# Kernel optimization log

Hardware: AMD Instinct MI355X
Metric: run time of the kernel (lower is better)

## Reference

```python
import jax, jax.numpy as jnp
import numpy as np

EPS = 1e-5

def rmsnorm(x):
    # BitLinear pre-norm (no learnable scale), per BitNet b1.58 reference impl
    return x * jax.lax.rsqrt(jnp.mean(x * x, axis=-1, keepdims=True) + EPS)

def act_quant(x):
    # per-token absmax 8-bit quantization with straight-through estimator
    scale = 127.0 / jnp.clip(jnp.max(jnp.abs(x), axis=-1, keepdims=True), 1e-5)
    q = jnp.clip(jnp.round(x * scale), -128.0, 127.0) / scale
    return x + jax.lax.stop_gradient(q - x)

def weight_quant(w):
    # absmean ternary quantization {-1,0,1} with STE
    scale = 1.0 / jnp.clip(jnp.mean(jnp.abs(w)), 1e-5)
    q = jnp.clip(jnp.round(w * scale), -1.0, 1.0) / scale
    return w + jax.lax.stop_gradient(q - w)

def bitlinear(x, w, b):
    # x: [b, s, d_in], w: [d_out, d_in] (torch Linear layout), b: [d_out]
    xq = act_quant(rmsnorm(x))
    wq = weight_quant(w)
    return jnp.einsum('bsd,fd->bsf', xq, wq) + b

def setup_inputs() -> dict:
    key = jax.random.key(0)
    k0, k1, k2 = jax.random.split(key, 3)
    B, S, D, F = 2, 8192, 1024, 4096  # inner_dim = dim * mult = 4096
    x = jax.random.normal(k0, (B, S, D), dtype=jnp.float32)
    w1 = jax.random.normal(k1, (F, D), dtype=jnp.float32) * (1.0 / np.sqrt(D))
    b1 = jnp.zeros((F,), dtype=jnp.float32)
    w2 = jax.random.normal(k2, (D, F), dtype=jnp.float32) * (1.0 / np.sqrt(F))
    b2 = jnp.zeros((D,), dtype=jnp.float32)
    return {"x": x, "w1": w1, "b1": b1, "w2": w2, "b2": b2}

def reference(x, w1, b1, w2, b2):
    h = bitlinear(x, w1, b1)
    h = jax.nn.gelu(h, approximate=False)  # nn.GELU() default is exact
    # post_act_ln=False -> no LayerNorm; dropout p=0.0 -> identity
    return bitlinear(h, w2, b2)
```

## Files before the change

kernel.cpp:

```cpp
#include <hip/hip_runtime.h>
#include <hip/hip_bf16.h>
#include <stdint.h>

typedef int i32x4 __attribute__((ext_vector_type(4)));

__device__ __forceinline__ float blo(unsigned int u) {
  unsigned int v = u << 16; float f; __builtin_memcpy(&f, &v, 4); return f;
}
__device__ __forceinline__ float bhi(unsigned int u) {
  unsigned int v = u & 0xffff0000u; float f; __builtin_memcpy(&f, &v, 4); return f;
}
__device__ __forceinline__ int pack4q(float a, float b, float c, float d, float qm) {
  int i0 = (int)rintf(a * qm) & 255;
  int i1 = (int)rintf(b * qm) & 255;
  int i2 = (int)rintf(c * qm) & 255;
  int i3 = (int)rintf(d * qm) & 255;
  return i0 | (i1 << 8) | (i2 << 16) | (i3 << 24);
}

__device__ __forceinline__ float fast_gelu(float v) {
  float u = v * 0.70710678118654752f;
  float s = fabsf(u);
  float den = fmaf(0.3275911f, s, 1.0f);
  float t;
  asm("v_rcp_f32 %0, %1" : "=v"(t) : "v"(den));
  float p = t * fmaf(t, fmaf(t, fmaf(t, fmaf(t, 1.061405429f, -1.453152027f),
                                     1.421413741f), -0.284496736f), 0.254829592f);
  float e = fmaf(-p, __expf(-u * u), 1.0f);
  float er = copysignf(e, u);
  return 0.5f * v * (1.0f + er);
}

__global__ void k_reduce_abs2(const float* __restrict__ w1, const float* __restrict__ w2,
                              long n4, float* __restrict__ partials) {
  const int half = gridDim.x >> 1;
  const float* w = (blockIdx.x < half) ? w1 : w2;
  int b = (blockIdx.x < half) ? blockIdx.x : blockIdx.x - half;
  const float4* wv = (const float4*)w;
  float s = 0.0f;
  long stride = (long)half * blockDim.x;
  for (long i = (long)b * blockDim.x + threadIdx.x; i < n4; i += stride) {
    float4 v = wv[i];
    s += fabsf(v.x) + fabsf(v.y) + fabsf(v.z) + fabsf(v.w);
  }
  #pragma unroll
  for (int off = 32; off; off >>= 1) s += __shfl_down(s, off);
  __shared__ float sw[4];
  if ((threadIdx.x & 63) == 0) sw[threadIdx.x >> 6] = s;
  __syncthreads();
  if (threadIdx.x == 0) partials[blockIdx.x] = sw[0] + sw[1] + sw[2] + sw[3];
}

__global__ void k_finalize_scales(const float* __restrict__ p1, const float* __restrict__ p2,
                                  float* __restrict__ scales, float inv1, float inv2) {
  int t = threadIdx.x;
  float s1 = p1[t], s2 = p2[t];
  #pragma unroll
  for (int off = 32; off; off >>= 1) { s1 += __shfl_down(s1, off); s2 += __shfl_down(s2, off); }
  __shared__ float a1[4], a2[4];
  if ((t & 63) == 0) { a1[t >> 6] = s1; a2[t >> 6] = s2; }
  __syncthreads();
  if (t == 0) {
    scales[0] = fmaxf((a1[0]+a1[1]+a1[2]+a1[3]) * inv1, 1e-5f);
    scales[1] = fmaxf((a2[0]+a2[1]+a2[2]+a2[3]) * inv2, 1e-5f);
  }
}

__global__ void k_quant_w2(const float* __restrict__ w1, char* __restrict__ wq1,
                           const float* __restrict__ w2, char* __restrict__ wq2,
                           long n4, const float* __restrict__ scales) {
  const int half = gridDim.x >> 1;
  const bool first = blockIdx.x < half;
  const float* w = first ? w1 : w2;
  char* wq = first ? wq1 : wq2;
  int b = first ? blockIdx.x : blockIdx.x - half;
  float s = 1.0f / scales[first ? 0 : 1];
  const float4* wv = (const float4*)w;
  int* qv = (int*)wq;
  long stride = (long)half * blockDim.x;
  for (long i = (long)b * blockDim.x + threadIdx.x; i < n4; i += stride) {
    float4 v = wv[i];
    int b0 = (int)fminf(fmaxf(rintf(v.x * s), -1.0f), 1.0f) & 255;
    int b1 = (int)fminf(fmaxf(rintf(v.y * s), -1.0f), 1.0f) & 255;
    int b2 = (int)fminf(fmaxf(rintf(v.z * s), -1.0f), 1.0f) & 255;
    int b3 = (int)fminf(fmaxf(rintf(v.w * s), -1.0f), 1.0f) & 255;
    qv[i] = b0 | (b1 << 8) | (b2 << 16) | (b3 << 24);
  }
}

__global__ void k_actq_x(const float* __restrict__ x, char* __restrict__ xq,
                         float* __restrict__ alpha) {
  const int D = 1024;
  size_t t = blockIdx.x;
  int tid = threadIdx.x;
  const float4* row = (const float4*)(x + t * (size_t)D);
  float4 v = row[tid];
  float ss = v.x*v.x + v.y*v.y + v.z*v.z + v.w*v.w;
  float am = fmaxf(fmaxf(fabsf(v.x), fabsf(v.y)), fmaxf(fabsf(v.z), fabsf(v.w)));
  #pragma unroll
  for (int off = 32; off; off >>= 1) {
    ss += __shfl_down(ss, off);
    am = fmaxf(am, __shfl_down(am, off));
  }
  __shared__ float s_ss[4], s_am[4];
  if ((tid & 63) == 0) { s_ss[tid >> 6] = ss; s_am[tid >> 6] = am; }
  __syncthreads();
  ss = s_ss[0] + s_ss[1] + s_ss[2] + s_ss[3];
  am = fmaxf(fmaxf(s_am[0], s_am[1]), fmaxf(s_am[2], s_am[3]));
  float rms = rsqrtf(ss * (1.0f / D) + 1e-5f);
  float a   = fmaxf(am * rms, 1e-5f);
  float qs  = 127.0f / a;
  if (tid == 0) alpha[t] = a * (1.0f / 127.0f);
  int b0 = (int)fminf(fmaxf(rintf((v.x * rms) * qs), -128.0f), 127.0f) & 255;
  int b1 = (int)fminf(fmaxf(rintf((v.y * rms) * qs), -128.0f), 127.0f) & 255;
  int b2 = (int)fminf(fmaxf(rintf((v.z * rms) * qs), -128.0f), 127.0f) & 255;
  int b3 = (int)fminf(fmaxf(rintf((v.w * rms) * qs), -128.0f), 127.0f) & 255;
  ((int*)xq)[t * 256 + tid] = b0 | (b1 << 8) | (b2 << 16) | (b3 << 24);
}

__global__ void k_actq_h(__hip_bfloat16* __restrict__ h, float* __restrict__ alpha) {
  const int F = 4096;
  size_t t = blockIdx.x;
  int tid = threadIdx.x;
  char* rb = (char*)(h + t * (size_t)F);
  const uint4* row = (const uint4*)rb;
  uint4 u0 = row[tid], u1 = row[tid + 256];
  unsigned int uu[8] = {u0.x, u0.y, u0.z, u0.w, u1.x, u1.y, u1.z, u1.w};
  float f[16];
  #pragma unroll
  for (int i = 0; i < 8; i++) {
    f[2*i]   = fast_gelu(blo(uu[i]));
    f[2*i+1] = fast_gelu(bhi(uu[i]));
  }
  float ss = 0.0f, am = 0.0f;
  #pragma unroll
  for (int i = 0; i < 16; i++) { ss += f[i] * f[i]; am = fmaxf(am, fabsf(f[i])); }
  #pragma unroll
  for (int off = 32; off; off >>= 1) {
    ss += __shfl_down(ss, off);
    am = fmaxf(am, __shfl_down(am, off));
  }
  __shared__ float s_ss[4], s_am[4];
  if ((tid & 63) == 0) { s_ss[tid >> 6] = ss; s_am[tid >> 6] = am; }
  __syncthreads();
  ss = s_ss[0] + s_ss[1] + s_ss[2] + s_ss[3];
  am = fmaxf(fmaxf(s_am[0], s_am[1]), fmaxf(s_am[2], s_am[3]));
  float rms = rsqrtf(ss * (1.0f / F) + 1e-5f);
  float a   = fmaxf(am * rms, 1e-5f);
  float qm  = rms * (127.0f / a);
  if (tid == 0) alpha[t] = a * (1.0f / 127.0f);
  uint2 w0, w1;
  w0.x = (unsigned)pack4q(f[0],  f[1],  f[2],  f[3],  qm);
  w0.y = (unsigned)pack4q(f[4],  f[5],  f[6],  f[7],  qm);
  w1.x = (unsigned)pack4q(f[8],  f[9],  f[10], f[11], qm);
  w1.y = (unsigned)pack4q(f[12], f[13], f[14], f[15], qm);
  *(uint2*)(rb + 8 * tid) = w0;
  *(uint2*)(rb + 2048 + 8 * tid) = w1;
}

#define GLD16(GP, LP) __builtin_amdgcn_global_load_lds( \
    (__attribute__((address_space(1))) void*)(GP), \
    (__attribute__((address_space(3))) void*)(LP), 16, 0, 0)
#define VMCNT3 asm volatile("s_waitcnt vmcnt(3)" ::: "memory")
#define VMCNT0 asm volatile("s_waitcnt vmcnt(0)" ::: "memory")
#define LGKM0  do { asm volatile("s_waitcnt lgkmcnt(0)" ::: "memory"); __builtin_amdgcn_sched_barrier(0); } while(0)

template<int EPI>
__global__ __launch_bounds__(512, 4) void k_gemm_i8(
    const char* __restrict__ A, int lda,
    const char* __restrict__ B,
    const float* __restrict__ bias, const float* __restrict__ alpha,
    const float* __restrict__ scales, int which,
    void* __restrict__ Cout, int N, int K, int lgnbx)
{
  __shared__ __align__(16) char lA[3 * 8192];
  __shared__ __align__(16) char lB[3 * 16384];
  const int tid = threadIdx.x, lane = tid & 63, wid = tid >> 6;
  const int wm = wid >> 2, wn = wid & 3;
  const int nwg = gridDim.x, bid = blockIdx.x;
  const int swz = (bid & 7) * (nwg >> 3) + (bid >> 3);
  const int bx = swz & ((1 << lgnbx) - 1), by = swz >> lgnbx;
  const int m0 = by * 128, n0 = bx * 256;
  const int NT = K >> 6;

  const int srow = tid >> 2, slot = tid & 3;
  const int sswz = (slot ^ ((srow >> 1) & 3)) * 16;
  const char* gA0 = A + (size_t)(m0 +       srow) * lda + sswz;
  const char* gB0 = B + (size_t)(n0 +       srow) * K   + sswz;
  const char* gB1 = B + (size_t)(n0 + 128 + srow) * K   + sswz;
  const int ldst = srow * 64 + slot * 16;

  const int lr = lane & 15;
  const int kx = ((lane >> 4) ^ ((lane >> 1) & 3)) * 16;
  const int aoff = (wm * 64 + lr) * 64 + kx;
  const int boff = (wn * 64 + lr) * 64 + kx;

  GLD16(gA0,      lA + ldst);
  GLD16(gB0,      lB + ldst);
  GLD16(gB1,      lB + 8192 + ldst);
  GLD16(gA0 + 64, lA + 8192 + ldst);
  GLD16(gB0 + 64, lB + 16384 + ldst);
  GLD16(gB1 + 64, lB + 16384 + 8192 + ldst);

  i32x4 acc[4][4] = {};
  int cur = 0, nx1 = 1, nx2 = 2;
  for (int t = 0; t < NT; ++t) {
    const bool pf = (t + 2 < NT);
    if (t + 1 < NT) { VMCNT3; } else { VMCNT0; }
    __builtin_amdgcn_s_barrier();
    const char* pa = lA + cur * 8192 + aoff;
    const char* pb = lB + cur * 16384 + boff;
    i32x4 av[4], bv[4];
    {
      av[0] = *(const i32x4*)(pa);
      av[1] = *(const i32x4*)(pa + 1024);
      #pragma unroll
      for (int n = 0; n < 4; ++n) bv[n] = *(const i32x4*)(pb + n * 1024);
      if (pf) {
        GLD16(gA0 + 64 * (t + 2), lA + nx2 * 8192 + ldst);
        GLD16(gB0 + 64 * (t + 2), lB + nx2 * 16384 + ldst);
      }
      __builtin_amdgcn_s_barrier();
      LGKM0;
      __builtin_amdgcn_s_setprio(1);
      #pragma unroll
      for (int j = 0; j < 2; ++j)
        #pragma unroll
        for (int n = 0; n < 4; ++n)
          acc[j][n] = __builtin_amdgcn_mfma_i32_16x16x64_i8(av[j], bv[n], acc[j][n], 0, 0, 0);
      __builtin_amdgcn_s_setprio(0);
      __builtin_amdgcn_s_barrier();
    }
    {
      av[2] = *(const i32x4*)(pa + 2048);
      av[3] = *(const i32x4*)(pa + 3072);
      if (pf) GLD16(gB1 + 64 * (t + 2), lB + nx2 * 16384 + 8192 + ldst);
      LGKM0;
      __builtin_amdgcn_s_setprio(1);
      #pragma unroll
      for (int j = 2; j < 4; ++j)
        #pragma unroll
        for (int n = 0; n < 4; ++n)
          acc[j][n] = __builtin_amdgcn_mfma_i32_16x16x64_i8(av[j], bv[n], acc[j][n], 0, 0, 0);
      __builtin_amdgcn_s_setprio(0);
    }
    int tmp = cur; cur = nx1; nx1 = nx2; nx2 = tmp;
  }

  const float wdq = scales[which];
  const int lq4 = (lane >> 4) * 4;
  #pragma unroll
  for (int m = 0; m < 4; ++m) {
    const int rowb = m0 + wm * 64 + m * 16 + lq4;
    float al[4];
    #pragma unroll
    for (int q = 0; q < 4; ++q) al[q] = alpha[rowb + q] * wdq;
    #pragma unroll
    for (int n = 0; n < 4; ++n) {
      const int col = n0 + wn * 64 + n * 16 + lr;
      const float bb = bias[col];
      #pragma unroll
      for (int q = 0; q < 4; ++q) {
        float v = (float)acc[m][n][q] * al[q] + bb;
        if constexpr (EPI == 0) {
          ((__hip_bfloat16*)Cout)[(size_t)(rowb + q) * N + col] = __float2bfloat16(v);
        } else {
          ((float*)Cout)[(size_t)(rowb + q) * N + col] = v;
        }
      }
    }
  }
}

extern "C" void kernel_launch(void* const* d_in, const int* in_sizes, int n_in,
                              void* d_out, int out_size, void* d_ws, size_t ws_size,
                              hipStream_t stream) {
  const float* x  = (const float*)d_in[0];
  const float* w1 = (const float*)d_in[1];
  const float* b1 = (const float*)d_in[2];
  const float* w2 = (const float*)d_in[3];
  const float* b2 = (const float*)d_in[4];
  const int  F = in_sizes[2];
  const int  D = in_sizes[4];
  const long T = (long)in_sizes[0] / D;
  const long nW = (long)F * D;

  char* ws = (char*)d_ws;
  float* partials = (float*)ws;
  float* scales   = partials + 512;
  float* alpha1 = (float*)(ws + 4096);
  float* alpha2 = alpha1 + T;
  size_t off = 4096 + 2 * (size_t)T * sizeof(float);
  off = (off + 255) & ~(size_t)255;
  char* w1q = ws + off; off += (size_t)nW;
  char* w2q = ws + off; off += (size_t)nW;
  char* xq  = ws + off; off += (size_t)T * D;
  off = (off + 255) & ~(size_t)255;
  __hip_bfloat16* h = (__hip_bfloat16*)(ws + off); off += (size_t)T * F * 2;
  if (ws_size < off) return;

  float invW = (float)(1.0 / (double)nW);
  k_reduce_abs2<<<512, 256, 0, stream>>>(w1, w2, nW / 4, partials);
  k_finalize_scales<<<1, 256, 0, stream>>>(partials, partials + 256, scales, invW, invW);
  k_quant_w2<<<4096, 256, 0, stream>>>(w1, w1q, w2, w2q, nW / 4, scales);
  k_actq_x<<<(unsigned)T, 256, 0, stream>>>(x, xq, alpha1);

  dim3 g1((unsigned)((T / 128) * (F / 256)));
  k_gemm_i8<0><<<g1, 512, 0, stream>>>(xq, D, w1q, b1, alpha1, scales, 0,
                                       h, F, D, __builtin_ctz(F / 256));

  k_actq_h<<<(unsigned)T, 256, 0, stream>>>(h, alpha2);

  dim3 g2((unsigned)((T / 128) * (D / 256)));
  k_gemm_i8<1><<<g2, 512, 0, stream>>>((const char*)h, F * 2, w2q, b2, alpha2, scales, 1,
                                       (float*)d_out, D, F, __builtin_ctz(D / 256));
}
```

Before: 254.8 us.

## Simplify second GEMM main loop and use 512-thread blocks for hidden quantization

The second GEMM (EPI==1) now uses a single-phase loop body. It issues all three prefetches for stage t+2 first, loads all A/B fragments, waits once, and runs all 16 MFMAs. This replaces the two-half schedule with its extra intra-iteration barriers. The hidden-activation GELU+quant kernel now runs 512 threads per row, each handling 8 bf16 values instead of 16, with an 8-wave shared reduction. The aim is fewer barriers in the K=4096 GEMM and more parallelism in the elementwise pass, at the cost of less interleaving of LDS reads with MFMAs.

```diff
diff --git a/kernel.cpp b/kernel.cpp
--- a/kernel.cpp
+++ b/kernel.cpp
@@ -123,39 +123,36 @@
   size_t t = blockIdx.x;
   int tid = threadIdx.x;
   char* rb = (char*)(h + t * (size_t)F);
-  const uint4* row = (const uint4*)rb;
-  uint4 u0 = row[tid], u1 = row[tid + 256];
-  unsigned int uu[8] = {u0.x, u0.y, u0.z, u0.w, u1.x, u1.y, u1.z, u1.w};
-  float f[16];
-  #pragma unroll
-  for (int i = 0; i < 8; i++) {
+  uint4 u = ((const uint4*)rb)[tid];
+  unsigned int uu[4] = {u.x, u.y, u.z, u.w};
+  float f[8];
+  #pragma unroll
+  for (int i = 0; i < 4; i++) {
     f[2*i]   = fast_gelu(blo(uu[i]));
     f[2*i+1] = fast_gelu(bhi(uu[i]));
   }
   float ss = 0.0f, am = 0.0f;
   #pragma unroll
-  for (int i = 0; i < 16; i++) { ss += f[i] * f[i]; am = fmaxf(am, fabsf(f[i])); }
+  for (int i = 0; i < 8; i++) { ss += f[i] * f[i]; am = fmaxf(am, fabsf(f[i])); }
   #pragma unroll
   for (int off = 32; off; off >>= 1) {
     ss += __shfl_down(ss, off);
     am = fmaxf(am, __shfl_down(am, off));
   }
-  __shared__ float s_ss[4], s_am[4];
+  __shared__ float s_ss[8], s_am[8];
   if ((tid & 63) == 0) { s_ss[tid >> 6] = ss; s_am[tid >> 6] = am; }
   __syncthreads();
-  ss = s_ss[0] + s_ss[1] + s_ss[2] + s_ss[3];
-  am = fmaxf(fmaxf(s_am[0], s_am[1]), fmaxf(s_am[2], s_am[3]));
+  ss = 0.0f; am = 0.0f;
+  #pragma unroll
+  for (int i = 0; i < 8; i++) { ss += s_ss[i]; am = fmaxf(am, s_am[i]); }
   float rms = rsqrtf(ss * (1.0f / F) + 1e-5f);
   float a   = fmaxf(am * rms, 1e-5f);
   float qm  = rms * (127.0f / a);
   if (tid == 0) alpha[t] = a * (1.0f / 127.0f);
-  uint2 w0, w1;
-  w0.x = (unsigned)pack4q(f[0],  f[1],  f[2],  f[3],  qm);
-  w0.y = (unsigned)pack4q(f[4],  f[5],  f[6],  f[7],  qm);
-  w1.x = (unsigned)pack4q(f[8],  f[9],  f[10], f[11], qm);
-  w1.y = (unsigned)pack4q(f[12], f[13], f[14], f[15], qm);
+  uint2 w0;
+  w0.x = (unsigned)pack4q(f[0], f[1], f[2], f[3], qm);
+  w0.y = (unsigned)pack4q(f[4], f[5], f[6], f[7], qm);
   *(uint2*)(rb + 8 * tid) = w0;
-  *(uint2*)(rb + 2048 + 8 * tid) = w1;
 }
 
 #define GLD16(GP, LP) __builtin_amdgcn_global_load_lds( \
@@ -211,7 +208,7 @@
     const char* pa = lA + cur * 8192 + aoff;
     const char* pb = lB + cur * 16384 + boff;
     i32x4 av[4], bv[4];
-    {
+    if constexpr (EPI == 0) {
       av[0] = *(const i32x4*)(pa);
       av[1] = *(const i32x4*)(pa + 1024);
       #pragma unroll
@@ -230,8 +227,6 @@
           acc[j][n] = __builtin_amdgcn_mfma_i32_16x16x64_i8(av[j], bv[n], acc[j][n], 0, 0, 0);
       __builtin_amdgcn_s_setprio(0);
       __builtin_amdgcn_s_barrier();
-    }
-    {
       av[2] = *(const i32x4*)(pa + 2048);
       av[3] = *(const i32x4*)(pa + 3072);
       if (pf) GLD16(gB1 + 64 * (t + 2), lB + nx2 * 16384 + 8192 + ldst);
@@ -239,6 +234,24 @@
       __builtin_amdgcn_s_setprio(1);
       #pragma unroll
       for (int j = 2; j < 4; ++j)
+        #pragma unroll
+        for (int n = 0; n < 4; ++n)
+          acc[j][n] = __builtin_amdgcn_mfma_i32_16x16x64_i8(av[j], bv[n], acc[j][n], 0, 0, 0);
+      __builtin_amdgcn_s_setprio(0);
+    } else {
+      if (pf) {
+        GLD16(gA0 + 64 * (t + 2), lA + nx2 * 8192 + ldst);
+        GLD16(gB0 + 64 * (t + 2), lB + nx2 * 16384 + ldst);
+        GLD16(gB1 + 64 * (t + 2), lB + nx2 * 16384 + 8192 + ldst);
+      }
+      #pragma unroll
+      for (int j = 0; j < 4; ++j) av[j] = *(const i32x4*)(pa + j * 1024);
+      #pragma unroll
+      for (int n = 0; n < 4; ++n) bv[n] = *(const i32x4*)(pb + n * 1024);
+      LGKM0;
+      __builtin_amdgcn_s_setprio(1);
+      #pragma unroll
+      for (int j = 0; j < 4; ++j)
         #pragma unroll
         for (int n = 0; n < 4; ++n)
           acc[j][n] = __builtin_amdgcn_mfma_i32_16x16x64_i8(av[j], bv[n], acc[j][n], 0, 0, 0);
@@ -309,7 +322,7 @@
   k_gemm_i8<0><<<g1, 512, 0, stream>>>(xq, D, w1q, b1, alpha1, scales, 0,
                                        h, F, D, __builtin_ctz(F / 256));
 
-  k_actq_h<<<(unsigned)T, 256, 0, stream>>>(h, alpha2);
+  k_actq_h<<<(unsigned)T, 512, 0, stream>>>(h, alpha2);
 
   dim3 g2((unsigned)((T / 128) * (D / 256)));
   k_gemm_i8<1><<<g2, 512, 0, stream>>>((const char*)h, F * 2, w2q, b2, alpha2, scales, 1,
```

New measurement: 259.2 us. About the same (+1.7%).
